# Optimization experiments

Measured on AMD Instinct MI355X. Metric: run time of the kernel, lower is better.

## Reference

```python
import jax, jax.numpy as jnp
import numpy as np

NUM_HEADS = 8
SPARSITY = 0.7


def setup_inputs() -> dict:
    key = jax.random.key(0)
    k1, k2, k3, k4, k5 = jax.random.split(key, 5)
    B, N, C = 4, 2048, 256
    return {
        "x": jax.random.normal(k1, (B, N, C), dtype=jnp.float32),
        "w_qkv": jax.random.normal(k2, (3 * C, C), dtype=jnp.float32) * (C ** -0.5),
        "b_qkv": jax.random.normal(k3, (3 * C,), dtype=jnp.float32) * 0.02,
        "w_proj": jax.random.normal(k4, (C, C), dtype=jnp.float32) * (C ** -0.5),
        "b_proj": jax.random.normal(k5, (C,), dtype=jnp.float32) * 0.02,
    }


def reference(x, w_qkv, b_qkv, w_proj, b_proj):
    B, N, C = x.shape
    H = NUM_HEADS
    D = C // H
    scale = D ** -0.5
    # qkv projection (torch Linear: x @ W.T + b)
    qkv = x @ w_qkv.T + b_qkv                      # [B, N, 3C]
    qkv = qkv.reshape(B, N, 3, H, D).transpose(2, 0, 3, 1, 4)  # [3, B, H, N, D]
    q, k, v = qkv[0], qkv[1], qkv[2]
    attn = jnp.einsum('bhnd,bhmd->bhnm', q, k) * scale  # [B, H, N, N]
    # dynamic per-row top-k threshold mask (note: zeros out logits, not -inf,
    # faithfully matching the original torch code)
    num_keep = int(N * (1.0 - SPARSITY))
    topk_vals = jax.lax.top_k(attn, num_keep)[0]        # [B, H, N, num_keep]
    threshold = topk_vals[..., -1:]                      # k-th largest per row
    mask = (attn >= threshold).astype(attn.dtype)
    attn = attn * mask
    attn = jax.nn.softmax(attn, axis=-1)
    out = jnp.einsum('bhnm,bhmd->bhnd', attn, v)         # [B, H, N, D]
    out = out.transpose(0, 2, 1, 3).reshape(B, N, C)
    return out @ w_proj.T + b_proj
```

## Files before the change

kernel.cpp:

```cpp
#include <hip/hip_runtime.h>

#define BDIM 4
#define NSEQ 2048
#define CDIM 256
#define NHEADS 8
#define QB 4
#define NT2 32
#define NKEEP 614
#define SSTR 2056
#define ATTN_SCALE 0.17677669529663688f

__global__ __launch_bounds__(256) void gemm_nt_bias(
    const float* __restrict__ A, const float* __restrict__ W,
    const float* __restrict__ bias, float* __restrict__ C,
    int M, int Nt, int K)
{
    __shared__ __align__(16) float As[32][68];
    __shared__ __align__(16) float Ws[32][68];
    const int tid = threadIdx.x;
    const int bm = blockIdx.x * 64;
    const int bn = blockIdx.y * 64;
    const int tm = tid >> 4;
    const int tn = tid & 15;
    const int lr = tid >> 2;
    const int lq = tid & 3;
    const float* Ap = A + (size_t)(bm + lr) * K + lq * 8;
    const float* Wp = W + (size_t)(bn + lr) * K + lq * 8;
    float acc[4][4] = {};

    for (int k0 = 0; k0 < K; k0 += 32) {
        float4 a0 = *(const float4*)(Ap + k0);
        float4 a1 = *(const float4*)(Ap + k0 + 4);
        float4 w0 = *(const float4*)(Wp + k0);
        float4 w1 = *(const float4*)(Wp + k0 + 4);
        __syncthreads();
        const int kq = lq * 8;
        As[kq+0][lr]=a0.x; As[kq+1][lr]=a0.y; As[kq+2][lr]=a0.z; As[kq+3][lr]=a0.w;
        As[kq+4][lr]=a1.x; As[kq+5][lr]=a1.y; As[kq+6][lr]=a1.z; As[kq+7][lr]=a1.w;
        Ws[kq+0][lr]=w0.x; Ws[kq+1][lr]=w0.y; Ws[kq+2][lr]=w0.z; Ws[kq+3][lr]=w0.w;
        Ws[kq+4][lr]=w1.x; Ws[kq+5][lr]=w1.y; Ws[kq+6][lr]=w1.z; Ws[kq+7][lr]=w1.w;
        __syncthreads();
        #pragma unroll
        for (int k = 0; k < 32; ++k) {
            float4 av = *(const float4*)&As[k][tm*4];
            float4 wv = *(const float4*)&Ws[k][tn*4];
            acc[0][0] += av.x*wv.x; acc[0][1] += av.x*wv.y; acc[0][2] += av.x*wv.z; acc[0][3] += av.x*wv.w;
            acc[1][0] += av.y*wv.x; acc[1][1] += av.y*wv.y; acc[1][2] += av.y*wv.z; acc[1][3] += av.y*wv.w;
            acc[2][0] += av.z*wv.x; acc[2][1] += av.z*wv.y; acc[2][2] += av.z*wv.z; acc[2][3] += av.z*wv.w;
            acc[3][0] += av.w*wv.x; acc[3][1] += av.w*wv.y; acc[3][2] += av.w*wv.z; acc[3][3] += av.w*wv.w;
        }
    }
    float4 bb = *(const float4*)(bias + bn + tn*4);
    #pragma unroll
    for (int i = 0; i < 4; ++i) {
        float4 o;
        o.x = acc[i][0] + bb.x;
        o.y = acc[i][1] + bb.y;
        o.z = acc[i][2] + bb.z;
        o.w = acc[i][3] + bb.w;
        *(float4*)(C + (size_t)(bm + tm*4 + i) * Nt + bn + tn*4) = o;
    }
}

__device__ __forceinline__ unsigned int f2key(float f) {
    unsigned int u = __float_as_uint(f);
    return (u & 0x80000000u) ? ~u : (u | 0x80000000u);
}

__device__ __forceinline__ float dpp_xor1_add(float x) {
    int s = __builtin_amdgcn_mov_dpp(__float_as_int(x), 0xB1, 0xF, 0xF, true);
    return x + __int_as_float(s);
}
__device__ __forceinline__ float dpp_xor2_add(float x) {
    int s = __builtin_amdgcn_mov_dpp(__float_as_int(x), 0x4E, 0xF, 0xF, true);
    return x + __int_as_float(s);
}

#define RBAR() do { asm volatile("s_waitcnt lgkmcnt(0)" ::: "memory"); \
                    __builtin_amdgcn_s_barrier();                      \
                    asm volatile("" ::: "memory"); } while (0)
#define LGKM0() asm volatile("s_waitcnt lgkmcnt(0)" ::: "memory")

__global__ __launch_bounds__(256, 4) void sparse_attn(
    const float* __restrict__ qkv, float* __restrict__ aout)
{
    __shared__ __align__(16) float  sbuf[QB * SSTR];
    __shared__ __align__(16) unsigned int hist[QB * 256];
    __shared__ unsigned int prefS[QB];
    __shared__ int   remS[QB];
    __shared__ float zS[QB];

    const int tid = threadIdx.x;
    const int w   = tid >> 6;
    const int l   = tid & 63;
    const int p   = l & 3;
    const int jg  = l >> 2;

    const int blk = blockIdx.x;
    const int nqb = NSEQ / QB;
    const int bh  = blk / nqb;
    const int qblk = blk % nqb;
    const int b = bh / NHEADS, h = bh % NHEADS;
    const int n0 = qblk * QB;

    const float* base = qkv + (size_t)b * NSEQ * 768;
    const float* kptr = base + 256 + h * 32 + p * 8 + (size_t)((w << 9) + jg) * 768;
    const float* vptr = base + 512 + h * 32 + p * 8 + (size_t)((w << 9) + jg) * 768;
#define KADDR(t) (kptr + (size_t)(t) * (16 * 768))
#define VADDR(t) (vptr + (size_t)(t) * (16 * 768))

    float4 qa[QB], qc[QB];
    {
        const float* gq = base + (size_t)n0 * 768 + h * 32 + p * 8;
        #pragma unroll
        for (int r = 0; r < QB; ++r) {
            float4 x0 = *(const float4*)(gq + (size_t)r * 768);
            float4 x1 = *(const float4*)(gq + (size_t)r * 768 + 4);
            qa[r].x = x0.x * ATTN_SCALE; qa[r].y = x0.y * ATTN_SCALE;
            qa[r].z = x0.z * ATTN_SCALE; qa[r].w = x0.w * ATTN_SCALE;
            qc[r].x = x1.x * ATTN_SCALE; qc[r].y = x1.y * ATTN_SCALE;
            qc[r].z = x1.z * ATTN_SCALE; qc[r].w = x1.w * ATTN_SCALE;
        }
    }
    {
        uint4 z4; z4.x = 0u; z4.y = 0u; z4.z = 0u; z4.w = 0u;
        *(uint4*)(hist + tid * 4) = z4;
    }
    if (tid < QB) { prefS[tid] = 0u; remS[tid] = NKEEP; }
    RBAR();

#define QK_TILE(K0, K1, T) do {                                               \
        float sc0 = qa[0].x*(K0).x + qa[0].y*(K0).y + qa[0].z*(K0).z + qa[0].w*(K0).w \
                  + qc[0].x*(K1).x + qc[0].y*(K1).y + qc[0].z*(K1).z + qc[0].w*(K1).w; \
        float sc1 = qa[1].x*(K0).x + qa[1].y*(K0).y + qa[1].z*(K0).z + qa[1].w*(K0).w \
                  + qc[1].x*(K1).x + qc[1].y*(K1).y + qc[1].z*(K1).z + qc[1].w*(K1).w; \
        float sc2 = qa[2].x*(K0).x + qa[2].y*(K0).y + qa[2].z*(K0).z + qa[2].w*(K0).w \
                  + qc[2].x*(K1).x + qc[2].y*(K1).y + qc[2].z*(K1).z + qc[2].w*(K1).w; \
        float sc3 = qa[3].x*(K0).x + qa[3].y*(K0).y + qa[3].z*(K0).z + qa[3].w*(K0).w \
                  + qc[3].x*(K1).x + qc[3].y*(K1).y + qc[3].z*(K1).z + qc[3].w*(K1).w; \
        sc0 = dpp_xor2_add(dpp_xor1_add(sc0));                                \
        sc1 = dpp_xor2_add(dpp_xor1_add(sc1));                                \
        sc2 = dpp_xor2_add(dpp_xor1_add(sc2));                                \
        sc3 = dpp_xor2_add(dpp_xor1_add(sc3));                                \
        float myv = (p == 0) ? sc0 : (p == 1) ? sc1 : (p == 2) ? sc2 : sc3;   \
        const int col = (w << 9) + ((T) << 4) + jg;                           \
        sbuf[p * SSTR + col] = myv;                                           \
        atomicAdd(&hist[p * 256 + (f2key(myv) >> 24)], 1u);                   \
    } while (0)

    float4 ka0 = *(const float4*)(KADDR(0)), ka1 = *(const float4*)(KADDR(0) + 4);
    float4 kb0 = *(const float4*)(KADDR(1)), kb1 = *(const float4*)(KADDR(1) + 4);
    float4 kc0 = *(const float4*)(KADDR(2)), kc1 = *(const float4*)(KADDR(2) + 4);
    float4 kd0 = *(const float4*)(KADDR(3)), kd1 = *(const float4*)(KADDR(3) + 4);
    #pragma unroll 1
    for (int t = 0; t < NT2; t += 4) {
        float4 c0, c1;
        c0 = ka0; c1 = ka1;
        if (t + 4 < NT2) { ka0 = *(const float4*)(KADDR(t + 4)); ka1 = *(const float4*)(KADDR(t + 4) + 4); }
        QK_TILE(c0, c1, t);
        c0 = kb0; c1 = kb1;
        if (t + 5 < NT2) { kb0 = *(const float4*)(KADDR(t + 5)); kb1 = *(const float4*)(KADDR(t + 5) + 4); }
        QK_TILE(c0, c1, t + 1);
        c0 = kc0; c1 = kc1;
        if (t + 6 < NT2) { kc0 = *(const float4*)(KADDR(t + 6)); kc1 = *(const float4*)(KADDR(t + 6) + 4); }
        QK_TILE(c0, c1, t + 2);
        c0 = kd0; c1 = kd1;
        if (t + 7 < NT2) { kd0 = *(const float4*)(KADDR(t + 7)); kd1 = *(const float4*)(KADDR(t + 7) + 4); }
        QK_TILE(c0, c1, t + 3);
    }
    float4 va0 = *(const float4*)(VADDR(0)), va1 = *(const float4*)(VADDR(0) + 4);
    float4 vb0 = *(const float4*)(VADDR(1)), vb1 = *(const float4*)(VADDR(1) + 4);
    float4 vc0 = *(const float4*)(VADDR(2)), vc1 = *(const float4*)(VADDR(2) + 4);
    float4 vd0 = *(const float4*)(VADDR(3)), vd1 = *(const float4*)(VADDR(3) + 4);
    RBAR();

    unsigned int* hrow = hist + w * 256;
    #pragma unroll 1
    for (int pass = 3; pass >= 0; --pass) {
        const int sh = pass * 8;
        const unsigned int pr = prefS[w];
        const int remv = remS[w];
        if (pass != 3) {
            const unsigned int hmsk = 0xFFFFFFFFu << (sh + 8);
            uint4 z4; z4.x = 0u; z4.y = 0u; z4.z = 0u; z4.w = 0u;
            *(uint4*)(hrow + l * 4) = z4;
            LGKM0();
            #pragma unroll 2
            for (int e = 0; e < 8; ++e) {
                float4 v = *(const float4*)&sbuf[w * SSTR + l * 4 + 256 * e];
                unsigned int k0 = f2key(v.x), k1 = f2key(v.y), k2 = f2key(v.z), k3 = f2key(v.w);
                if ((k0 & hmsk) == pr) atomicAdd(&hrow[(k0 >> sh) & 255u], 1u);
                if ((k1 & hmsk) == pr) atomicAdd(&hrow[(k1 >> sh) & 255u], 1u);
                if ((k2 & hmsk) == pr) atomicAdd(&hrow[(k2 >> sh) & 255u], 1u);
                if ((k3 & hmsk) == pr) atomicAdd(&hrow[(k3 >> sh) & 255u], 1u);
            }
            LGKM0();
        }
        uint4 c4 = *(const uint4*)(hrow + l * 4);
        unsigned int cnt[4] = { c4.x, c4.y, c4.z, c4.w };
        unsigned int part = cnt[0] + cnt[1] + cnt[2] + cnt[3];
        unsigned int suf = part;
        #pragma unroll
        for (int dlt = 1; dlt < 64; dlt <<= 1) {
            unsigned int v = __shfl_down(suf, dlt);
            if (l + dlt < 64) suf += v;
        }
        unsigned int run = suf - part;
        #pragma unroll
        for (int i = 3; i >= 0; --i) {
            if ((int)run < remv && remv <= (int)(run + cnt[i])) {
                remS[w]  = remv - (int)run;
                prefS[w] = pr | ((unsigned int)(l * 4 + i) << sh);
            }
            run += cnt[i];
        }
        LGKM0();
    }

    {
        unsigned int key = prefS[w];
        unsigned int u = (key & 0x80000000u) ? (key & 0x7FFFFFFFu) : ~key;
        const float thr = __uint_as_float(u);
        float mx = 0.f;
        #pragma unroll 2
        for (int e = 0; e < 8; ++e) {
            float* sp = &sbuf[w * SSTR + l * 4 + 256 * e];
            float4 v = *(const float4*)sp;
            v.x = (v.x >= thr) ? v.x : 0.f;
            v.y = (v.y >= thr) ? v.y : 0.f;
            v.z = (v.z >= thr) ? v.z : 0.f;
            v.w = (v.w >= thr) ? v.w : 0.f;
            *(float4*)sp = v;
            mx = fmaxf(mx, fmaxf(fmaxf(v.x, v.y), fmaxf(v.z, v.w)));
        }
        #pragma unroll
        for (int d2 = 32; d2 >= 1; d2 >>= 1) mx = fmaxf(mx, __shfl_xor(mx, d2));
        float Z = 0.f;
        const float cm = __expf(0.f - mx);
        if (thr > 0.f) {
            #pragma unroll 2
            for (int e = 0; e < 8; ++e) {
                float* sp = &sbuf[w * SSTR + l * 4 + 256 * e];
                float4 v = *(const float4*)sp;
                v.x = (v.x > 0.f) ? __expf(v.x - mx) : cm;
                v.y = (v.y > 0.f) ? __expf(v.y - mx) : cm;
                v.z = (v.z > 0.f) ? __expf(v.z - mx) : cm;
                v.w = (v.w > 0.f) ? __expf(v.w - mx) : cm;
                *(float4*)sp = v;
                Z += v.x + v.y + v.z + v.w;
            }
        } else {
            #pragma unroll 2
            for (int e = 0; e < 8; ++e) {
                float* sp = &sbuf[w * SSTR + l * 4 + 256 * e];
                float4 v = *(const float4*)sp;
                v.x = __expf(v.x - mx); v.y = __expf(v.y - mx);
                v.z = __expf(v.z - mx); v.w = __expf(v.w - mx);
                *(float4*)sp = v;
                Z += v.x + v.y + v.z + v.w;
            }
        }
        #pragma unroll
        for (int d2 = 32; d2 >= 1; d2 >>= 1) Z += __shfl_xor(Z, d2);
        if (l == 0) zS[w] = Z;
    }
    RBAR();

    float4 oa0, oa1, oa2, oa3, ob0, ob1, ob2, ob3;
    oa0.x=0;oa0.y=0;oa0.z=0;oa0.w=0; ob0=oa0; oa1=oa0; ob1=oa0;
    oa2=oa0; ob2=oa0; oa3=oa0; ob3=oa0;

#define PV_TILE(V0, V1, T) do {                                               \
        const int col = (w << 9) + ((T) << 4) + jg;                           \
        float p0 = sbuf[0 * SSTR + col];                                      \
        float p1 = sbuf[1 * SSTR + col];                                      \
        float p2 = sbuf[2 * SSTR + col];                                      \
        float p3 = sbuf[3 * SSTR + col];                                      \
        oa0.x=fmaf(p0,(V0).x,oa0.x); oa0.y=fmaf(p0,(V0).y,oa0.y); oa0.z=fmaf(p0,(V0).z,oa0.z); oa0.w=fmaf(p0,(V0).w,oa0.w); \
        ob0.x=fmaf(p0,(V1).x,ob0.x); ob0.y=fmaf(p0,(V1).y,ob0.y); ob0.z=fmaf(p0,(V1).z,ob0.z); ob0.w=fmaf(p0,(V1).w,ob0.w); \
        oa1.x=fmaf(p1,(V0).x,oa1.x); oa1.y=fmaf(p1,(V0).y,oa1.y); oa1.z=fmaf(p1,(V0).z,oa1.z); oa1.w=fmaf(p1,(V0).w,oa1.w); \
        ob1.x=fmaf(p1,(V1).x,ob1.x); ob1.y=fmaf(p1,(V1).y,ob1.y); ob1.z=fmaf(p1,(V1).z,ob1.z); ob1.w=fmaf(p1,(V1).w,ob1.w); \
        oa2.x=fmaf(p2,(V0).x,oa2.x); oa2.y=fmaf(p2,(V0).y,oa2.y); oa2.z=fmaf(p2,(V0).z,oa2.z); oa2.w=fmaf(p2,(V0).w,oa2.w); \
        ob2.x=fmaf(p2,(V1).x,ob2.x); ob2.y=fmaf(p2,(V1).y,ob2.y); ob2.z=fmaf(p2,(V1).z,ob2.z); ob2.w=fmaf(p2,(V1).w,ob2.w); \
        oa3.x=fmaf(p3,(V0).x,oa3.x); oa3.y=fmaf(p3,(V0).y,oa3.y); oa3.z=fmaf(p3,(V0).z,oa3.z); oa3.w=fmaf(p3,(V0).w,oa3.w); \
        ob3.x=fmaf(p3,(V1).x,ob3.x); ob3.y=fmaf(p3,(V1).y,ob3.y); ob3.z=fmaf(p3,(V1).z,ob3.z); ob3.w=fmaf(p3,(V1).w,ob3.w); \
    } while (0)

    #pragma unroll 1
    for (int t = 0; t < NT2; t += 4) {
        float4 c0, c1;
        c0 = va0; c1 = va1;
        if (t + 4 < NT2) { va0 = *(const float4*)(VADDR(t + 4)); va1 = *(const float4*)(VADDR(t + 4) + 4); }
        PV_TILE(c0, c1, t);
        c0 = vb0; c1 = vb1;
        if (t + 5 < NT2) { vb0 = *(const float4*)(VADDR(t + 5)); vb1 = *(const float4*)(VADDR(t + 5) + 4); }
        PV_TILE(c0, c1, t + 1);
        c0 = vc0; c1 = vc1;
        if (t + 6 < NT2) { vc0 = *(const float4*)(VADDR(t + 6)); vc1 = *(const float4*)(VADDR(t + 6) + 4); }
        PV_TILE(c0, c1, t + 2);
        c0 = vd0; c1 = vd1;
        if (t + 7 < NT2) { vd0 = *(const float4*)(VADDR(t + 7)); vd1 = *(const float4*)(VADDR(t + 7) + 4); }
        PV_TILE(c0, c1, t + 3);
    }
    RBAR();

    #pragma unroll
    for (int d2 = 4; d2 <= 32; d2 <<= 1) {
        oa0.x+=__shfl_xor(oa0.x,d2); oa0.y+=__shfl_xor(oa0.y,d2); oa0.z+=__shfl_xor(oa0.z,d2); oa0.w+=__shfl_xor(oa0.w,d2);
        ob0.x+=__shfl_xor(ob0.x,d2); ob0.y+=__shfl_xor(ob0.y,d2); ob0.z+=__shfl_xor(ob0.z,d2); ob0.w+=__shfl_xor(ob0.w,d2);
        oa1.x+=__shfl_xor(oa1.x,d2); oa1.y+=__shfl_xor(oa1.y,d2); oa1.z+=__shfl_xor(oa1.z,d2); oa1.w+=__shfl_xor(oa1.w,d2);
        ob1.x+=__shfl_xor(ob1.x,d2); ob1.y+=__shfl_xor(ob1.y,d2); ob1.z+=__shfl_xor(ob1.z,d2); ob1.w+=__shfl_xor(ob1.w,d2);
        oa2.x+=__shfl_xor(oa2.x,d2); oa2.y+=__shfl_xor(oa2.y,d2); oa2.z+=__shfl_xor(oa2.z,d2); oa2.w+=__shfl_xor(oa2.w,d2);
        ob2.x+=__shfl_xor(ob2.x,d2); ob2.y+=__shfl_xor(ob2.y,d2); ob2.z+=__shfl_xor(ob2.z,d2); ob2.w+=__shfl_xor(ob2.w,d2);
        oa3.x+=__shfl_xor(oa3.x,d2); oa3.y+=__shfl_xor(oa3.y,d2); oa3.z+=__shfl_xor(oa3.z,d2); oa3.w+=__shfl_xor(oa3.w,d2);
        ob3.x+=__shfl_xor(ob3.x,d2); ob3.y+=__shfl_xor(ob3.y,d2); ob3.z+=__shfl_xor(ob3.z,d2); ob3.w+=__shfl_xor(ob3.w,d2);
    }
    if (l < 4) {
        float* part = &sbuf[0];
        *(float4*)&part[(w * 4 + 0) * 32 + l * 8]     = oa0;
        *(float4*)&part[(w * 4 + 0) * 32 + l * 8 + 4] = ob0;
        *(float4*)&part[(w * 4 + 1) * 32 + l * 8]     = oa1;
        *(float4*)&part[(w * 4 + 1) * 32 + l * 8 + 4] = ob1;
        *(float4*)&part[(w * 4 + 2) * 32 + l * 8]     = oa2;
        *(float4*)&part[(w * 4 + 2) * 32 + l * 8 + 4] = ob2;
        *(float4*)&part[(w * 4 + 3) * 32 + l * 8]     = oa3;
        *(float4*)&part[(w * 4 + 3) * 32 + l * 8 + 4] = ob3;
    }
    RBAR();
    if (tid < 128) {
        const int r = tid >> 5, d = tid & 31;
        const float* part = &sbuf[0];
        float o = part[(0 * 4 + r) * 32 + d] + part[(1 * 4 + r) * 32 + d]
                + part[(2 * 4 + r) * 32 + d] + part[(3 * 4 + r) * 32 + d];
        o /= zS[r];
        aout[((size_t)b * NSEQ + n0 + r) * CDIM + h * 32 + d] = o;
    }
}

extern "C" void kernel_launch(void* const* d_in, const int* in_sizes, int n_in,
                              void* d_out, int out_size, void* d_ws, size_t ws_size,
                              hipStream_t stream) {
    (void)in_sizes; (void)n_in; (void)out_size; (void)ws_size;
    const float* x      = (const float*)d_in[0];
    const float* w_qkv  = (const float*)d_in[1];
    const float* b_qkv  = (const float*)d_in[2];
    const float* w_proj = (const float*)d_in[3];
    const float* b_proj = (const float*)d_in[4];
    float* out = (float*)d_out;

    const int M = BDIM * NSEQ;
    float* qkv_ws  = (float*)d_ws;
    float* attn_ws = qkv_ws + (size_t)M * 768;

    dim3 g1(M / 64, 768 / 64);
    gemm_nt_bias<<<g1, 256, 0, stream>>>(x, w_qkv, b_qkv, qkv_ws, M, 768, 256);

    sparse_attn<<<BDIM * NHEADS * (NSEQ / QB), 256, 0, stream>>>(qkv_ws, attn_ws);

    dim3 g2(M / 64, 256 / 64);
    gemm_nt_bias<<<g2, 256, 0, stream>>>(attn_ws, w_proj, b_proj, out, M, 256, 256);
}
```

Before: 653.8 us.

## Gather only kept keys for PV and fold masked entries via V column sums

The softmax over masked logits is split algebraically: every masked position contributes exp(-mx), so its share of P·V is cm times the column sum of V, which a new small kernel precomputes per (batch, head). Each wave compacts the indices of kept keys with ballot/mbcnt into a shared index buffer, then gathers only those V rows (about 30% of keys) and applies exp-minus-cm weights. This removes the dense PV pass and the extra softmax write-back sweeps. The radix-select histograms are also packed as 16-bit counters two per word. The trade-offs are an extra launch, scattered V row gathers, and a CAP=640 cap that silently drops keys when ties push the kept count past it.

After: 953.5 us. 1.46x slower.

```diff
diff --git a/kernel.cpp b/kernel.cpp
--- a/kernel.cpp
+++ b/kernel.cpp
@@ -8,7 +8,12 @@
 #define NT2 32
 #define NKEEP 614
 #define SSTR 2056
+#define CAP 640
 #define ATTN_SCALE 0.17677669529663688f
+
+typedef unsigned long long ull;
+
+__device__ float colsumG[BDIM * NHEADS * 32];
 
 __global__ __launch_bounds__(256) void gemm_nt_bias(
     const float* __restrict__ A, const float* __restrict__ W,
@@ -62,11 +67,36 @@
     }
 }
 
+__global__ __launch_bounds__(256) void vcolsum(const float* __restrict__ qkv)
+{
+    const int bh = blockIdx.x;
+    const int bb = bh >> 3, hh = bh & 7;
+    const int g = threadIdx.x >> 5, d = threadIdx.x & 31;
+    const float* vp = qkv + (size_t)bb * NSEQ * 768 + 512 + hh * 32 + d;
+    const int nbase = g * 256;
+    float s0 = 0.f, s1 = 0.f, s2 = 0.f, s3 = 0.f;
+    #pragma unroll 4
+    for (int n = 0; n < 256; n += 4) {
+        s0 += vp[(size_t)(nbase + n    ) * 768];
+        s1 += vp[(size_t)(nbase + n + 1) * 768];
+        s2 += vp[(size_t)(nbase + n + 2) * 768];
+        s3 += vp[(size_t)(nbase + n + 3) * 768];
+    }
+    __shared__ float red[8][32];
+    red[g][d] = (s0 + s1) + (s2 + s3);
+    __syncthreads();
+    if (threadIdx.x < 32) {
+        float t = 0.f;
+        #pragma unroll
+        for (int gg = 0; gg < 8; ++gg) t += red[gg][threadIdx.x];
+        colsumG[bh * 32 + threadIdx.x] = t;
+    }
+}
+
 __device__ __forceinline__ unsigned int f2key(float f) {
     unsigned int u = __float_as_uint(f);
     return (u & 0x80000000u) ? ~u : (u | 0x80000000u);
 }
-
 __device__ __forceinline__ float dpp_xor1_add(float x) {
     int s = __builtin_amdgcn_mov_dpp(__float_as_int(x), 0xB1, 0xF, 0xF, true);
     return x + __int_as_float(s);
@@ -74,6 +104,10 @@
 __device__ __forceinline__ float dpp_xor2_add(float x) {
     int s = __builtin_amdgcn_mov_dpp(__float_as_int(x), 0x4E, 0xF, 0xF, true);
     return x + __int_as_float(s);
+}
+__device__ __forceinline__ unsigned lanecnt_lt(ull m) {
+    return __builtin_amdgcn_mbcnt_hi((unsigned)(m >> 32),
+           __builtin_amdgcn_mbcnt_lo((unsigned)(m & 0xFFFFFFFFull), 0u));
 }
 
 #define RBAR() do { asm volatile("s_waitcnt lgkmcnt(0)" ::: "memory"); \
@@ -84,11 +118,11 @@
 __global__ __launch_bounds__(256, 4) void sparse_attn(
     const float* __restrict__ qkv, float* __restrict__ aout)
 {
-    __shared__ __align__(16) float  sbuf[QB * SSTR];
-    __shared__ __align__(16) unsigned int hist[QB * 256];
+    __shared__ __align__(16) float sbuf[QB * SSTR];
+    __shared__ __align__(16) unsigned int histw[QB * 128];
+    __shared__ __align__(16) unsigned short idxb[QB * CAP];
     __shared__ unsigned int prefS[QB];
-    __shared__ int   remS[QB];
-    __shared__ float zS[QB];
+    __shared__ int remS[QB];
 
     const int tid = threadIdx.x;
     const int w   = tid >> 6;
@@ -105,9 +139,7 @@
 
     const float* base = qkv + (size_t)b * NSEQ * 768;
     const float* kptr = base + 256 + h * 32 + p * 8 + (size_t)((w << 9) + jg) * 768;
-    const float* vptr = base + 512 + h * 32 + p * 8 + (size_t)((w << 9) + jg) * 768;
 #define KADDR(t) (kptr + (size_t)(t) * (16 * 768))
-#define VADDR(t) (vptr + (size_t)(t) * (16 * 768))
 
     float4 qa[QB], qc[QB];
     {
@@ -122,10 +154,7 @@
             qc[r].z = x1.z * ATTN_SCALE; qc[r].w = x1.w * ATTN_SCALE;
         }
     }
-    {
-        uint4 z4; z4.x = 0u; z4.y = 0u; z4.z = 0u; z4.w = 0u;
-        *(uint4*)(hist + tid * 4) = z4;
-    }
+    ((uint2*)histw)[tid] = make_uint2(0u, 0u);
     if (tid < QB) { prefS[tid] = 0u; remS[tid] = NKEEP; }
     RBAR();
 
@@ -145,7 +174,8 @@
         float myv = (p == 0) ? sc0 : (p == 1) ? sc1 : (p == 2) ? sc2 : sc3;   \
         const int col = (w << 9) + ((T) << 4) + jg;                           \
         sbuf[p * SSTR + col] = myv;                                           \
-        atomicAdd(&hist[p * 256 + (f2key(myv) >> 24)], 1u);                   \
+        unsigned kk = f2key(myv);                                             \
+        atomicAdd(&histw[p * 128 + (kk >> 25)], 1u << (((kk >> 24) & 1u) * 16)); \
     } while (0)
 
     float4 ka0 = *(const float4*)(KADDR(0)), ka1 = *(const float4*)(KADDR(0) + 4);
@@ -168,13 +198,10 @@
         if (t + 7 < NT2) { kd0 = *(const float4*)(KADDR(t + 7)); kd1 = *(const float4*)(KADDR(t + 7) + 4); }
         QK_TILE(c0, c1, t + 3);
     }
-    float4 va0 = *(const float4*)(VADDR(0)), va1 = *(const float4*)(VADDR(0) + 4);
-    float4 vb0 = *(const float4*)(VADDR(1)), vb1 = *(const float4*)(VADDR(1) + 4);
-    float4 vc0 = *(const float4*)(VADDR(2)), vc1 = *(const float4*)(VADDR(2) + 4);
-    float4 vd0 = *(const float4*)(VADDR(3)), vd1 = *(const float4*)(VADDR(3) + 4);
     RBAR();
 
-    unsigned int* hrow = hist + w * 256;
+    const int myrowbase = w * SSTR;
+    unsigned int* hroww = histw + w * 128;
     #pragma unroll 1
     for (int pass = 3; pass >= 0; --pass) {
         const int sh = pass * 8;
@@ -182,22 +209,21 @@
         const int remv = remS[w];
         if (pass != 3) {
             const unsigned int hmsk = 0xFFFFFFFFu << (sh + 8);
-            uint4 z4; z4.x = 0u; z4.y = 0u; z4.z = 0u; z4.w = 0u;
-            *(uint4*)(hrow + l * 4) = z4;
+            *(uint2*)(hroww + 2 * l) = make_uint2(0u, 0u);
             LGKM0();
             #pragma unroll 2
             for (int e = 0; e < 8; ++e) {
-                float4 v = *(const float4*)&sbuf[w * SSTR + l * 4 + 256 * e];
+                float4 v = *(const float4*)&sbuf[myrowbase + l * 4 + 256 * e];
                 unsigned int k0 = f2key(v.x), k1 = f2key(v.y), k2 = f2key(v.z), k3 = f2key(v.w);
-                if ((k0 & hmsk) == pr) atomicAdd(&hrow[(k0 >> sh) & 255u], 1u);
-                if ((k1 & hmsk) == pr) atomicAdd(&hrow[(k1 >> sh) & 255u], 1u);
-                if ((k2 & hmsk) == pr) atomicAdd(&hrow[(k2 >> sh) & 255u], 1u);
-                if ((k3 & hmsk) == pr) atomicAdd(&hrow[(k3 >> sh) & 255u], 1u);
+                if ((k0 & hmsk) == pr) { unsigned bn = (k0 >> sh) & 255u; atomicAdd(&hroww[bn >> 1], 1u << ((bn & 1u) * 16)); }
+                if ((k1 & hmsk) == pr) { unsigned bn = (k1 >> sh) & 255u; atomicAdd(&hroww[bn >> 1], 1u << ((bn & 1u) * 16)); }
+                if ((k2 & hmsk) == pr) { unsigned bn = (k2 >> sh) & 255u; atomicAdd(&hroww[bn >> 1], 1u << ((bn & 1u) * 16)); }
+                if ((k3 & hmsk) == pr) { unsigned bn = (k3 >> sh) & 255u; atomicAdd(&hroww[bn >> 1], 1u << ((bn & 1u) * 16)); }
             }
             LGKM0();
         }
-        uint4 c4 = *(const uint4*)(hrow + l * 4);
-        unsigned int cnt[4] = { c4.x, c4.y, c4.z, c4.w };
+        uint2 cw = *(const uint2*)(hroww + 2 * l);
+        unsigned int cnt[4] = { cw.x & 0xFFFFu, cw.x >> 16, cw.y & 0xFFFFu, cw.y >> 16 };
         unsigned int part = cnt[0] + cnt[1] + cnt[2] + cnt[3];
         unsigned int suf = part;
         #pragma unroll
@@ -217,123 +243,114 @@
         LGKM0();
     }
 
+    float mx = 0.f;
+    unsigned int cbase = 0;
     {
         unsigned int key = prefS[w];
-        unsigned int u = (key & 0x80000000u) ? (key & 0x7FFFFFFFu) : ~key;
-        const float thr = __uint_as_float(u);
-        float mx = 0.f;
+        unsigned int uu = (key & 0x80000000u) ? (key & 0x7FFFFFFFu) : ~key;
+        const float thr = __uint_as_float(uu);
         #pragma unroll 2
         for (int e = 0; e < 8; ++e) {
-            float* sp = &sbuf[w * SSTR + l * 4 + 256 * e];
-            float4 v = *(const float4*)sp;
-            v.x = (v.x >= thr) ? v.x : 0.f;
-            v.y = (v.y >= thr) ? v.y : 0.f;
-            v.z = (v.z >= thr) ? v.z : 0.f;
-            v.w = (v.w >= thr) ? v.w : 0.f;
-            *(float4*)sp = v;
-            mx = fmaxf(mx, fmaxf(fmaxf(v.x, v.y), fmaxf(v.z, v.w)));
-        }
-        #pragma unroll
-        for (int d2 = 32; d2 >= 1; d2 >>= 1) mx = fmaxf(mx, __shfl_xor(mx, d2));
-        float Z = 0.f;
-        const float cm = __expf(0.f - mx);
-        if (thr > 0.f) {
-            #pragma unroll 2
-            for (int e = 0; e < 8; ++e) {
-                float* sp = &sbuf[w * SSTR + l * 4 + 256 * e];
-                float4 v = *(const float4*)sp;
-                v.x = (v.x > 0.f) ? __expf(v.x - mx) : cm;
-                v.y = (v.y > 0.f) ? __expf(v.y - mx) : cm;
-                v.z = (v.z > 0.f) ? __expf(v.z - mx) : cm;
-                v.w = (v.w > 0.f) ? __expf(v.w - mx) : cm;
-                *(float4*)sp = v;
-                Z += v.x + v.y + v.z + v.w;
-            }
-        } else {
-            #pragma unroll 2
-            for (int e = 0; e < 8; ++e) {
-                float* sp = &sbuf[w * SSTR + l * 4 + 256 * e];
-                float4 v = *(const float4*)sp;
-                v.x = __expf(v.x - mx); v.y = __expf(v.y - mx);
-                v.z = __expf(v.z - mx); v.w = __expf(v.w - mx);
-                *(float4*)sp = v;
-                Z += v.x + v.y + v.z + v.w;
-            }
-        }
-        #pragma unroll
-        for (int d2 = 32; d2 >= 1; d2 >>= 1) Z += __shfl_xor(Z, d2);
-        if (l == 0) zS[w] = Z;
-    }
-    RBAR();
-
-    float4 oa0, oa1, oa2, oa3, ob0, ob1, ob2, ob3;
-    oa0.x=0;oa0.y=0;oa0.z=0;oa0.w=0; ob0=oa0; oa1=oa0; ob1=oa0;
-    oa2=oa0; ob2=oa0; oa3=oa0; ob3=oa0;
-
-#define PV_TILE(V0, V1, T) do {                                               \
-        const int col = (w << 9) + ((T) << 4) + jg;                           \
-        float p0 = sbuf[0 * SSTR + col];                                      \
-        float p1 = sbuf[1 * SSTR + col];                                      \
-        float p2 = sbuf[2 * SSTR + col];                                      \
-        float p3 = sbuf[3 * SSTR + col];                                      \
-        oa0.x=fmaf(p0,(V0).x,oa0.x); oa0.y=fmaf(p0,(V0).y,oa0.y); oa0.z=fmaf(p0,(V0).z,oa0.z); oa0.w=fmaf(p0,(V0).w,oa0.w); \
-        ob0.x=fmaf(p0,(V1).x,ob0.x); ob0.y=fmaf(p0,(V1).y,ob0.y); ob0.z=fmaf(p0,(V1).z,ob0.z); ob0.w=fmaf(p0,(V1).w,ob0.w); \
-        oa1.x=fmaf(p1,(V0).x,oa1.x); oa1.y=fmaf(p1,(V0).y,oa1.y); oa1.z=fmaf(p1,(V0).z,oa1.z); oa1.w=fmaf(p1,(V0).w,oa1.w); \
-        ob1.x=fmaf(p1,(V1).x,ob1.x); ob1.y=fmaf(p1,(V1).y,ob1.y); ob1.z=fmaf(p1,(V1).z,ob1.z); ob1.w=fmaf(p1,(V1).w,ob1.w); \
-        oa2.x=fmaf(p2,(V0).x,oa2.x); oa2.y=fmaf(p2,(V0).y,oa2.y); oa2.z=fmaf(p2,(V0).z,oa2.z); oa2.w=fmaf(p2,(V0).w,oa2.w); \
-        ob2.x=fmaf(p2,(V1).x,ob2.x); ob2.y=fmaf(p2,(V1).y,ob2.y); ob2.z=fmaf(p2,(V1).z,ob2.z); ob2.w=fmaf(p2,(V1).w,ob2.w); \
-        oa3.x=fmaf(p3,(V0).x,oa3.x); oa3.y=fmaf(p3,(V0).y,oa3.y); oa3.z=fmaf(p3,(V0).z,oa3.z); oa3.w=fmaf(p3,(V0).w,oa3.w); \
-        ob3.x=fmaf(p3,(V1).x,ob3.x); ob3.y=fmaf(p3,(V1).y,ob3.y); ob3.z=fmaf(p3,(V1).z,ob3.z); ob3.w=fmaf(p3,(V1).w,ob3.w); \
+            float4 v = *(const float4*)&sbuf[myrowbase + l * 4 + 256 * e];
+            const int col0 = 256 * e + l * 4;
+            bool k0 = (v.x >= thr), k1 = (v.y >= thr), k2 = (v.z >= thr), k3 = (v.w >= thr);
+            mx = fmaxf(mx, fmaxf(fmaxf(k0 ? v.x : 0.f, k1 ? v.y : 0.f),
+                                 fmaxf(k2 ? v.z : 0.f, k3 ? v.w : 0.f)));
+            ull m;
+            m = __ballot(k0);
+            if (k0) { unsigned pos = cbase + lanecnt_lt(m); if (pos < CAP) idxb[w * CAP + pos] = (unsigned short)(col0 + 0); }
+            cbase += (unsigned)__popcll(m);
+            m = __ballot(k1);
+            if (k1) { unsigned pos = cbase + lanecnt_lt(m); if (pos < CAP) idxb[w * CAP + pos] = (unsigned short)(col0 + 1); }
+            cbase += (unsigned)__popcll(m);
+            m = __ballot(k2);
+            if (k2) { unsigned pos = cbase + lanecnt_lt(m); if (pos < CAP) idxb[w * CAP + pos] = (unsigned short)(col0 + 2); }
+            cbase += (unsigned)__popcll(m);
+            m = __ballot(k3);
+            if (k3) { unsigned pos = cbase + lanecnt_lt(m); if (pos < CAP) idxb[w * CAP + pos] = (unsigned short)(col0 + 3); }
+            cbase += (unsigned)__popcll(m);
+        }
+    }
+    #pragma unroll
+    for (int d2 = 32; d2 >= 1; d2 >>= 1) mx = fmaxf(mx, __shfl_xor(mx, d2));
+    const float cm = __expf(-mx);
+    const int L = (cbase < (unsigned)CAP) ? (int)cbase : CAP;
+    LGKM0();
+
+    const float* vbase = base + 512 + h * 32;
+    float4 A0, A1, A2, A3, A4, A5, A6, A7;
+    A0.x=0;A0.y=0;A0.z=0;A0.w=0; A1=A0;A2=A0;A3=A0;A4=A0;A5=A0;A6=A0;A7=A0;
+    float z = 0.f;
+    const int Lpad = (L + 63) & ~63;
+
+#define VGATH(X, vc) do {                                                        \
+        X##0 = *(const float4*)(vc);        X##1 = *(const float4*)((vc) + 4);   \
+        X##2 = *(const float4*)((vc) + 8);  X##3 = *(const float4*)((vc) + 12);  \
+        X##4 = *(const float4*)((vc) + 16); X##5 = *(const float4*)((vc) + 20);  \
+        X##6 = *(const float4*)((vc) + 24); X##7 = *(const float4*)((vc) + 28);  \
     } while (0)
-
+#define PVFMA(pp, X) do {                                                                                             \
+        A0.x=fmaf(pp,(X##0).x,A0.x); A0.y=fmaf(pp,(X##0).y,A0.y); A0.z=fmaf(pp,(X##0).z,A0.z); A0.w=fmaf(pp,(X##0).w,A0.w); \
+        A1.x=fmaf(pp,(X##1).x,A1.x); A1.y=fmaf(pp,(X##1).y,A1.y); A1.z=fmaf(pp,(X##1).z,A1.z); A1.w=fmaf(pp,(X##1).w,A1.w); \
+        A2.x=fmaf(pp,(X##2).x,A2.x); A2.y=fmaf(pp,(X##2).y,A2.y); A2.z=fmaf(pp,(X##2).z,A2.z); A2.w=fmaf(pp,(X##2).w,A2.w); \
+        A3.x=fmaf(pp,(X##3).x,A3.x); A3.y=fmaf(pp,(X##3).y,A3.y); A3.z=fmaf(pp,(X##3).z,A3.z); A3.w=fmaf(pp,(X##3).w,A3.w); \
+        A4.x=fmaf(pp,(X##4).x,A4.x); A4.y=fmaf(pp,(X##4).y,A4.y); A4.z=fmaf(pp,(X##4).z,A4.z); A4.w=fmaf(pp,(X##4).w,A4.w); \
+        A5.x=fmaf(pp,(X##5).x,A5.x); A5.y=fmaf(pp,(X##5).y,A5.y); A5.z=fmaf(pp,(X##5).z,A5.z); A5.w=fmaf(pp,(X##5).w,A5.w); \
+        A6.x=fmaf(pp,(X##6).x,A6.x); A6.y=fmaf(pp,(X##6).y,A6.y); A6.z=fmaf(pp,(X##6).z,A6.z); A6.w=fmaf(pp,(X##6).w,A6.w); \
+        A7.x=fmaf(pp,(X##7).x,A7.x); A7.y=fmaf(pp,(X##7).y,A7.y); A7.z=fmaf(pp,(X##7).z,A7.z); A7.w=fmaf(pp,(X##7).w,A7.w); \
+    } while (0)
+
+    bool actA = l < L;
+    int idxA = idxb[w * CAP + (actA ? l : 0)];
+    float svA = sbuf[myrowbase + idxA];
+    float4 xA0, xA1, xA2, xA3, xA4, xA5, xA6, xA7;
+    { const float* vcA = vbase + (size_t)idxA * 768; VGATH(xA, vcA); }
     #pragma unroll 1
-    for (int t = 0; t < NT2; t += 4) {
-        float4 c0, c1;
-        c0 = va0; c1 = va1;
-        if (t + 4 < NT2) { va0 = *(const float4*)(VADDR(t + 4)); va1 = *(const float4*)(VADDR(t + 4) + 4); }
-        PV_TILE(c0, c1, t);
-        c0 = vb0; c1 = vb1;
-        if (t + 5 < NT2) { vb0 = *(const float4*)(VADDR(t + 5)); vb1 = *(const float4*)(VADDR(t + 5) + 4); }
-        PV_TILE(c0, c1, t + 1);
-        c0 = vc0; c1 = vc1;
-        if (t + 6 < NT2) { vc0 = *(const float4*)(VADDR(t + 6)); vc1 = *(const float4*)(VADDR(t + 6) + 4); }
-        PV_TILE(c0, c1, t + 2);
-        c0 = vd0; c1 = vd1;
-        if (t + 7 < NT2) { vd0 = *(const float4*)(VADDR(t + 7)); vd1 = *(const float4*)(VADDR(t + 7) + 4); }
-        PV_TILE(c0, c1, t + 3);
-    }
-    RBAR();
+    for (int i = l; i < Lpad; i += 128) {
+        const int ib = i + 64;
+        const bool actB = ib < L;
+        const int idxB = idxb[w * CAP + (actB ? ib : 0)];
+        const float svB = sbuf[myrowbase + idxB];
+        float4 xB0, xB1, xB2, xB3, xB4, xB5, xB6, xB7;
+        { const float* vcB = vbase + (size_t)idxB * 768; VGATH(xB, vcB); }
+        float ppA = actA ? (__expf(svA - mx) - cm) : 0.f;
+        z += ppA;
+        PVFMA(ppA, xA);
+        const int ia = i + 128;
+        actA = ia < L;
+        idxA = idxb[w * CAP + (actA ? ia : 0)];
+        svA = sbuf[myrowbase + idxA];
+        { const float* vcA = vbase + (size_t)idxA * 768; VGATH(xA, vcA); }
+        float ppB = actB ? (__expf(svB - mx) - cm) : 0.f;
+        z += ppB;
+        PVFMA(ppB, xB);
+    }
 
     #pragma unroll
-    for (int d2 = 4; d2 <= 32; d2 <<= 1) {
-        oa0.x+=__shfl_xor(oa0.x,d2); oa0.y+=__shfl_xor(oa0.y,d2); oa0.z+=__shfl_xor(oa0.z,d2); oa0.w+=__shfl_xor(oa0.w,d2);
-        ob0.x+=__shfl_xor(ob0.x,d2); ob0.y+=__shfl_xor(ob0.y,d2); ob0.z+=__shfl_xor(ob0.z,d2); ob0.w+=__shfl_xor(ob0.w,d2);
-        oa1.x+=__shfl_xor(oa1.x,d2); oa1.y+=__shfl_xor(oa1.y,d2); oa1.z+=__shfl_xor(oa1.z,d2); oa1.w+=__shfl_xor(oa1.w,d2);
-        ob1.x+=__shfl_xor(ob1.x,d2); ob1.y+=__shfl_xor(ob1.y,d2); ob1.z+=__shfl_xor(ob1.z,d2); ob1.w+=__shfl_xor(ob1.w,d2);
-        oa2.x+=__shfl_xor(oa2.x,d2); oa2.y+=__shfl_xor(oa2.y,d2); oa2.z+=__shfl_xor(oa2.z,d2); oa2.w+=__shfl_xor(oa2.w,d2);
-        ob2.x+=__shfl_xor(ob2.x,d2); ob2.y+=__shfl_xor(ob2.y,d2); ob2.z+=__shfl_xor(ob2.z,d2); ob2.w+=__shfl_xor(ob2.w,d2);
-        oa3.x+=__shfl_xor(oa3.x,d2); oa3.y+=__shfl_xor(oa3.y,d2); oa3.z+=__shfl_xor(oa3.z,d2); oa3.w+=__shfl_xor(oa3.w,d2);
-        ob3.x+=__shfl_xor(ob3.x,d2); ob3.y+=__shfl_xor(ob3.y,d2); ob3.z+=__shfl_xor(ob3.z,d2); ob3.w+=__shfl_xor(ob3.w,d2);
-    }
-    if (l < 4) {
-        float* part = &sbuf[0];
-        *(float4*)&part[(w * 4 + 0) * 32 + l * 8]     = oa0;
-        *(float4*)&part[(w * 4 + 0) * 32 + l * 8 + 4] = ob0;
-        *(float4*)&part[(w * 4 + 1) * 32 + l * 8]     = oa1;
-        *(float4*)&part[(w * 4 + 1) * 32 + l * 8 + 4] = ob1;
-        *(float4*)&part[(w * 4 + 2) * 32 + l * 8]     = oa2;
-        *(float4*)&part[(w * 4 + 2) * 32 + l * 8 + 4] = ob2;
-        *(float4*)&part[(w * 4 + 3) * 32 + l * 8]     = oa3;
-        *(float4*)&part[(w * 4 + 3) * 32 + l * 8 + 4] = ob3;
-    }
-    RBAR();
-    if (tid < 128) {
-        const int r = tid >> 5, d = tid & 31;
-        const float* part = &sbuf[0];
-        float o = part[(0 * 4 + r) * 32 + d] + part[(1 * 4 + r) * 32 + d]
-                + part[(2 * 4 + r) * 32 + d] + part[(3 * 4 + r) * 32 + d];
-        o /= zS[r];
-        aout[((size_t)b * NSEQ + n0 + r) * CDIM + h * 32 + d] = o;
+    for (int d2 = 1; d2 <= 32; d2 <<= 1) {
+        z += __shfl_xor(z, d2);
+        A0.x += __shfl_xor(A0.x, d2); A0.y += __shfl_xor(A0.y, d2); A0.z += __shfl_xor(A0.z, d2); A0.w += __shfl_xor(A0.w, d2);
+        A1.x += __shfl_xor(A1.x, d2); A1.y += __shfl_xor(A1.y, d2); A1.z += __shfl_xor(A1.z, d2); A1.w += __shfl_xor(A1.w, d2);
+        A2.x += __shfl_xor(A2.x, d2); A2.y += __shfl_xor(A2.y, d2); A2.z += __shfl_xor(A2.z, d2); A2.w += __shfl_xor(A2.w, d2);
+        A3.x += __shfl_xor(A3.x, d2); A3.y += __shfl_xor(A3.y, d2); A3.z += __shfl_xor(A3.z, d2); A3.w += __shfl_xor(A3.w, d2);
+        A4.x += __shfl_xor(A4.x, d2); A4.y += __shfl_xor(A4.y, d2); A4.z += __shfl_xor(A4.z, d2); A4.w += __shfl_xor(A4.w, d2);
+        A5.x += __shfl_xor(A5.x, d2); A5.y += __shfl_xor(A5.y, d2); A5.z += __shfl_xor(A5.z, d2); A5.w += __shfl_xor(A5.w, d2);
+        A6.x += __shfl_xor(A6.x, d2); A6.y += __shfl_xor(A6.y, d2); A6.z += __shfl_xor(A6.z, d2); A6.w += __shfl_xor(A6.w, d2);
+        A7.x += __shfl_xor(A7.x, d2); A7.y += __shfl_xor(A7.y, d2); A7.z += __shfl_xor(A7.z, d2); A7.w += __shfl_xor(A7.w, d2);
+    }
+    if (l < 32) {
+        float val = 0.f;
+#define PICK(q, Aq) \
+        if (l == 4*q+0) val = (Aq).x; \
+        if (l == 4*q+1) val = (Aq).y; \
+        if (l == 4*q+2) val = (Aq).z; \
+        if (l == 4*q+3) val = (Aq).w;
+        PICK(0, A0) PICK(1, A1) PICK(2, A2) PICK(3, A3)
+        PICK(4, A4) PICK(5, A5) PICK(6, A6) PICK(7, A7)
+#undef PICK
+        const float Zt = z + 2048.f * cm;
+        const float cs = colsumG[(b * NHEADS + h) * 32 + l];
+        aout[((size_t)b * NSEQ + n0 + w) * CDIM + h * 32 + l] = (val + cm * cs) / Zt;
     }
 }
 
@@ -355,6 +372,8 @@
     dim3 g1(M / 64, 768 / 64);
     gemm_nt_bias<<<g1, 256, 0, stream>>>(x, w_qkv, b_qkv, qkv_ws, M, 768, 256);
 
+    vcolsum<<<BDIM * NHEADS, 256, 0, stream>>>(qkv_ws);
+
     sparse_attn<<<BDIM * NHEADS * (NSEQ / QB), 256, 0, stream>>>(qkv_ws, attn_ws);
 
     dim3 g2(M / 64, 256 / 64);
```
